# Kernel tuning notes

Hardware: AMD Instinct MI355X
Metric: run time of the kernel (lower is better)

Reference implementation:

```python
import jax, jax.numpy as jnp
import numpy as np

PI = float(np.pi)
K_NEIGH = 10  # self.k = k + 1 with k=9


def xyz2sphere(xyz):
    # cartesian2polar: [rho, theta/pi, phi/(2pi)+0.5] along last dim
    rho = jnp.sqrt(jnp.sum(xyz * xyz, axis=-1, keepdims=True))
    rho_s = jnp.maximum(rho, 1e-8)
    theta = jnp.arccos(jnp.clip(xyz[..., 2:3] / rho_s, -1.0, 1.0)) / PI
    phi = jnp.arctan2(xyz[..., 1:2], xyz[..., 0:1]) / (2.0 * PI) + 0.5
    return jnp.concatenate([rho, theta, phi], axis=-1)


def group_by_umbrella(xyz, k):
    # xyz: [B,3,N] -> [B,N,K,3,3] umbrella triangles (K = k-1 neighbors)
    pts = jnp.transpose(xyz, (0, 2, 1))                       # [B,N,3]
    sq = jnp.sum(pts * pts, axis=-1)                          # [B,N]
    d = sq[:, :, None] + sq[:, None, :] - 2.0 * jnp.einsum('bnc,bmc->bnm', pts, pts)
    idx = jax.lax.top_k(-d, k)[1]                             # [B,N,k] nearest incl. self
    group = jax.vmap(lambda p, i: p[i])(pts, idx)[:, :, 1:]   # drop self -> [B,N,K,3]
    gnorm = group - pts[:, :, None, :]                        # centered neighbors
    phi = xyz2sphere(gnorm)[..., 2]                           # [B,N,K]
    order = jnp.argsort(phi, axis=-1)
    srt = jnp.take_along_axis(gnorm, order[..., None], axis=2)[:, :, :, None, :]  # [B,N,K,1,3]
    rolled = jnp.roll(srt, -1, axis=2)
    return jnp.concatenate([jnp.zeros_like(srt), srt, rolled], axis=3)  # [B,N,K,3,3]


def cal_normal(g):
    # g: [B,N,K,3(points),3(coord)] -> unit normals [B,N,K,3]
    v1 = g[..., 1, :] - g[..., 0, :]
    v2 = g[..., 2, :] - g[..., 0, :]
    n = jnp.cross(v1, v2)
    nrm = jnp.sqrt(jnp.sum(n * n, axis=-1, keepdims=True))
    un = n / jnp.maximum(nrm, 1e-10)
    pos = jnp.where(un[..., 0:1, 0] > 0, 1.0, -1.0)[..., None]  # per-group sign fix
    return un * pos


def bn(x, g, b, m, v, eps=1e-5):
    # inference-mode BatchNorm2d over channel dim of [B,C,K,N]
    inv = g / jnp.sqrt(v + eps)
    return x * inv[:, None, None] + (b - m * inv)[:, None, None]


def conv1x1(x, w, b=None):
    y = jnp.einsum('oc,bckn->bokn', w, x)
    return y if b is None else y + b[:, None, None]


def setup_inputs() -> dict:
    key = jax.random.key(0)
    ks = jax.random.split(key, 16)
    C = 9
    return {
        'x': jax.random.normal(ks[0], (8, 3, 4096), dtype=jnp.float32),
        'conv1_w': jax.random.normal(ks[1], (C, C), dtype=jnp.float32) * 0.3,
        'bn1_g': jax.random.uniform(ks[2], (C,), dtype=jnp.float32) + 0.5,
        'bn1_b': jax.random.normal(ks[3], (C,), dtype=jnp.float32) * 0.1,
        'bn1_m': jax.random.normal(ks[4], (C,), dtype=jnp.float32) * 0.1,
        'bn1_v': jax.random.uniform(ks[5], (C,), dtype=jnp.float32) + 0.5,
        'conv2_w': jax.random.normal(ks[6], (C, C), dtype=jnp.float32) * 0.3,
        'conv2_b': jax.random.normal(ks[7], (C,), dtype=jnp.float32) * 0.1,
        'bn2_g': jax.random.uniform(ks[8], (C,), dtype=jnp.float32) + 0.5,
        'bn2_b': jax.random.normal(ks[9], (C,), dtype=jnp.float32) * 0.1,
        'bn2_m': jax.random.normal(ks[10], (C,), dtype=jnp.float32) * 0.1,
        'bn2_v': jax.random.uniform(ks[11], (C,), dtype=jnp.float32) + 0.5,
        'conv3_w': jax.random.normal(ks[12], (C, C), dtype=jnp.float32) * 0.3,
        'conv3_b': jax.random.normal(ks[13], (C,), dtype=jnp.float32) * 0.1,
    }


def reference(x, conv1_w, bn1_g, bn1_b, bn1_m, bn1_v, conv2_w, conv2_b,
              bn2_g, bn2_b, bn2_m, bn2_v, conv3_w, conv3_b):
    xyz = x[:, :3, :]
    gp = group_by_umbrella(xyz, K_NEIGH)                      # [B,N,K,3,3]
    normal = jnp.nan_to_num(cal_normal(gp))                   # [B,N,K,3]
    center = jnp.nan_to_num(jnp.mean(gp, axis=-2))            # [B,N,K,3]
    polar = xyz2sphere(center)                                # [B,N,K,3]
    feat = jnp.concatenate([center, polar, normal], axis=-1)  # [B,N,K,9]
    feat = jnp.transpose(feat, (0, 3, 2, 1))                  # [B,9,K,N]
    h = jax.nn.relu(bn(conv1x1(feat, conv1_w), bn1_g, bn1_b, bn1_m, bn1_v))
    h = jax.nn.relu(bn(conv1x1(h, conv2_w, conv2_b), bn2_g, bn2_b, bn2_m, bn2_v))
    h = conv1x1(h, conv3_w, conv3_b)
    return jnp.sum(h, axis=2)                                 # aggregation='sum' -> [B,9,N]
```

## Files before the change

kernel.cpp:

```cpp
#include <hip/hip_runtime.h>
#include <math.h>

#define NB 8
#define NP 4096
#define TOPK 10
#define KNB 9
#define QPB 16
#define SLC 8
#define NT 4
#define TPTS 1024
#define QPT (TPTS / SLC)
#define QW 132
#define CHW (SLC * QW)
#define MST (SLC * TOPK + 1)

#define FINF 3.0e38f
#define PI_F 3.14159274101257324f

__global__ __launch_bounds__(128, 4)
void repsurf_fused(const float* __restrict__ x,
                   const float* __restrict__ cw1,
                   const float* __restrict__ bg1, const float* __restrict__ bb1,
                   const float* __restrict__ bm1, const float* __restrict__ bv1,
                   const float* __restrict__ cw2, const float* __restrict__ cb2,
                   const float* __restrict__ bg2, const float* __restrict__ bb2,
                   const float* __restrict__ bm2, const float* __restrict__ bv2,
                   const float* __restrict__ cw3, const float* __restrict__ cb3,
                   float* __restrict__ out)
{
    __shared__ __align__(16) float uS[3 * CHW];
    float* md   = uS;
    int*   mi   = (int*)(uS + QPB * MST);
    float* tile = uS;

    __shared__ __align__(16) float sW1[9 * 12];
    __shared__ __align__(16) float sW2[9 * 12];
    __shared__ __align__(16) float sW3[9 * 12];
    __shared__ float sSh1[9], sSh2[9], sSh3[9];

    const int t  = threadIdx.x;
    const int b  = blockIdx.x >> 8;
    const int qc = blockIdx.x & 255;
    const float* xb = x + (size_t)b * 3 * NP;

    if (t < 108) {
        int o = t / 12, c = t % 12;
        float w1v = 0.f, w2v = 0.f, w3v = 0.f;
        if (c < 9) {
            float iv1 = bg1[o] * rsqrtf(bv1[o] + 1e-5f);
            float iv2 = bg2[o] * rsqrtf(bv2[o] + 1e-5f);
            w1v = cw1[o * 9 + c] * iv1;
            w2v = cw2[o * 9 + c] * iv2;
            w3v = cw3[o * 9 + c];
        }
        sW1[t] = w1v; sW2[t] = w2v; sW3[t] = w3v;
        if (t < 9) {
            float iv1 = bg1[t] * rsqrtf(bv1[t] + 1e-5f);
            float iv2 = bg2[t] * rsqrtf(bv2[t] + 1e-5f);
            sSh1[t] = bb1[t] - bm1[t] * iv1;
            sSh2[t] = cb2[t] * iv2 + bb2[t] - bm2[t] * iv2;
            sSh3[t] = cb3[t];
        }
    }

    const int q  = t & (QPB - 1);
    const int s  = t >> 4;
    const int qi = qc * QPB + q;
    const float qx = xb[qi], qy = xb[NP + qi], qz = xb[2 * NP + qi];

    float dk[TOPK];
    int   ik[TOPK];
#pragma unroll
    for (int j = 0; j < TOPK; ++j) { dk[j] = FINF; ik[j] = 0x7fffffff; }

    float db0 = 0.f, db1 = 0.f;
    int   ib0 = 0,   ib1 = 0,   cnt = 0;

#define INSERTE(DD, II) do { \
        float _d = (DD); int _i = (II); \
        if (_d < dk[TOPK - 1]) { \
            dk[TOPK - 1] = _d; ik[TOPK - 1] = _i; \
            _Pragma("unroll") \
            for (int jj = TOPK - 1; jj > 0; --jj) { \
                if (dk[jj] < dk[jj - 1]) { \
                    float td = dk[jj]; dk[jj] = dk[jj - 1]; dk[jj - 1] = td; \
                    int ti = ik[jj]; ik[jj] = ik[jj - 1]; ik[jj - 1] = ti; } \
            } \
        } } while (0)

#define DRAIN() do { \
        if (cnt >= 2) INSERTE(db1, ib1); \
        if (cnt >= 1) INSERTE(db0, ib0); \
        cnt = 0; } while (0)

#define DOCAND(PX, PY, PZ, MIDX) do { \
        float dx = (PX) - qx, dy = (PY) - qy, dz = (PZ) - qz; \
        float d = fmaf(dx, dx, fmaf(dy, dy, dz * dz)); \
        if (d < dk[TOPK - 1]) { db1 = db0; ib1 = ib0; db0 = d; ib0 = (MIDX); cnt++; } \
        if (__any(cnt >= 2)) DRAIN(); \
    } while (0)

    for (int tt = 0; tt < NT; ++tt) {
        const float* src0 = xb + tt * TPTS;
#pragma unroll
        for (int r = 0; r < 6; ++r) {
            int f = r * 128 + t;
            int c = f >> 8;
            int o = f & 255;
            float4 v = *(const float4*)(src0 + c * NP + o * 4);
            ((float4*)tile)[c * 264 + (o >> 5) * 33 + (o & 31)] = v;
        }
        __syncthreads();

        const float4* tx4 = (const float4*)tile + s * 33;
        const float4* ty4 = (const float4*)tile + 264 + s * 33;
        const float4* tz4 = (const float4*)tile + 528 + s * 33;
        const int base_idx = tt * TPTS + s * QPT;
        for (int mm = 0; mm < QPT / 4; ++mm) {
            float4 X = tx4[mm];
            float4 Y = ty4[mm];
            float4 Z = tz4[mm];
            const int m0 = base_idx + mm * 4;
            DOCAND(X.x, Y.x, Z.x, m0 + 0);
            DOCAND(X.y, Y.y, Z.y, m0 + 1);
            DOCAND(X.z, Y.z, Z.z, m0 + 2);
            DOCAND(X.w, Y.w, Z.w, m0 + 3);
        }
        __syncthreads();
    }
    DRAIN();

    const int qb = q * MST;
#pragma unroll
    for (int j = 0; j < TOPK; ++j) {
        md[qb + s * TOPK + j] = dk[j];
        mi[qb + s * TOPK + j] = ik[j];
    }
    __syncthreads();

    if (t < QPB) {
        int ni[KNB];
        int p0 = 0, p1 = 0, p2 = 0, p3 = 0, p4 = 0, p5 = 0, p6 = 0, p7 = 0;
#pragma unroll
        for (int j = 0; j < TOPK; ++j) {
#define GETH(K) float d##K; int i##K; \
            { int pk = p##K; \
              if (pk < TOPK) { d##K = md[qb + K * TOPK + pk]; i##K = mi[qb + K * TOPK + pk]; } \
              else { d##K = FINF; i##K = 0x7fffffff; } }
            GETH(0) GETH(1) GETH(2) GETH(3) GETH(4) GETH(5) GETH(6) GETH(7)
#undef GETH
#define WIN(DA, IA, SA, DB, IB, SB, DO_, IO_, SO_) \
            bool w_##SO_ = ((DA) < (DB)) || ((DA) == (DB) && (IA) < (IB)); \
            float DO_ = w_##SO_ ? (DA) : (DB); \
            int IO_ = w_##SO_ ? (IA) : (IB); \
            int SO_ = w_##SO_ ? (SA) : (SB);
            WIN(d0, i0, 0, d1, i1, 1, dA, iA, sA)
            WIN(d2, i2, 2, d3, i3, 3, dB, iB, sB)
            WIN(d4, i4, 4, d5, i5, 5, dC, iC, sC)
            WIN(d6, i6, 6, d7, i7, 7, dD, iD, sD)
            WIN(dA, iA, sA, dB, iB, sB, dE, iE, sE)
            WIN(dC, iC, sC, dD, iD, sD, dF, iF, sF)
            WIN(dE, iE, sE, dF, iF, sF, dG, iG, sw)
            (void)dG; (void)iG;
#undef WIN
            if (j > 0) ni[j - 1] = iG;
            p0 += (sw == 0); p1 += (sw == 1); p2 += (sw == 2); p3 += (sw == 3);
            p4 += (sw == 4); p5 += (sw == 5); p6 += (sw == 6); p7 += (sw == 7);
        }

        float gx[KNB], gy[KNB], gz[KNB], kk[KNB];
#pragma unroll
        for (int j = 0; j < KNB; ++j) {
            int id = ni[j];
            gx[j] = xb[id] - qx;
            gy[j] = xb[NP + id] - qy;
            gz[j] = xb[2 * NP + id] - qz;
            kk[j] = atan2f(gy[j], gx[j]);
        }
#pragma unroll
        for (int pass = 0; pass < KNB - 1; ++pass) {
#pragma unroll
            for (int j = 0; j < KNB - 1 - pass; ++j) {
                if (kk[j + 1] < kk[j]) {
                    float tv;
                    tv = kk[j]; kk[j] = kk[j + 1]; kk[j + 1] = tv;
                    tv = gx[j]; gx[j] = gx[j + 1]; gx[j + 1] = tv;
                    tv = gy[j]; gy[j] = gy[j + 1]; gy[j + 1] = tv;
                    tv = gz[j]; gz[j] = gz[j + 1]; gz[j + 1] = tv;
                }
            }
        }

        float ux[KNB], uy[KNB], uz[KNB];
#pragma unroll
        for (int j = 0; j < KNB; ++j) {
            int j2 = (j + 1 == KNB) ? 0 : j + 1;
            float nx_ = gy[j] * gz[j2] - gz[j] * gy[j2];
            float ny_ = gz[j] * gx[j2] - gx[j] * gz[j2];
            float nz_ = gx[j] * gy[j2] - gy[j] * gx[j2];
            float l = sqrtf(nx_ * nx_ + ny_ * ny_ + nz_ * nz_);
            float inv = 1.0f / fmaxf(l, 1e-10f);
            ux[j] = nx_ * inv; uy[j] = ny_ * inv; uz[j] = nz_ * inv;
        }
        float sgn = (ux[0] > 0.0f) ? 1.0f : -1.0f;

        const float4* W1v = (const float4*)sW1;
        const float4* W2v = (const float4*)sW2;
        const float4* W3v = (const float4*)sW3;

#define DOT9(WV, O, V) ( \
        (WV)[(O)*3+0].x * (V)[0] + (WV)[(O)*3+0].y * (V)[1] + \
        (WV)[(O)*3+0].z * (V)[2] + (WV)[(O)*3+0].w * (V)[3] + \
        (WV)[(O)*3+1].x * (V)[4] + (WV)[(O)*3+1].y * (V)[5] + \
        (WV)[(O)*3+1].z * (V)[6] + (WV)[(O)*3+1].w * (V)[7] + \
        (WV)[(O)*3+2].x * (V)[8] )

        float acc[9];
#pragma unroll
        for (int o = 0; o < 9; ++o) acc[o] = 0.0f;

#pragma unroll
        for (int j = 0; j < KNB; ++j) {
            int j2 = (j + 1 == KNB) ? 0 : j + 1;
            float cx = (gx[j] + gx[j2]) * (1.0f / 3.0f);
            float cy = (gy[j] + gy[j2]) * (1.0f / 3.0f);
            float cz = (gz[j] + gz[j2]) * (1.0f / 3.0f);
            float rho = sqrtf(cx * cx + cy * cy + cz * cz);
            float rs  = fmaxf(rho, 1e-8f);
            float ct  = fminf(fmaxf(cz / rs, -1.0f), 1.0f);
            float th  = acosf(ct) / PI_F;
            float ph  = atan2f(cy, cx) / (2.0f * PI_F) + 0.5f;
            float f[9]  = {cx, cy, cz, rho, th, ph, ux[j] * sgn, uy[j] * sgn, uz[j] * sgn};
            float t1[9], t2[9];
#pragma unroll
            for (int o = 0; o < 9; ++o)
                t1[o] = fmaxf(DOT9(W1v, o, f) + sSh1[o], 0.0f);
#pragma unroll
            for (int o = 0; o < 9; ++o)
                t2[o] = fmaxf(DOT9(W2v, o, t1) + sSh2[o], 0.0f);
#pragma unroll
            for (int o = 0; o < 9; ++o)
                acc[o] += DOT9(W3v, o, t2);
        }

        float* ob = out + (size_t)b * 9 * NP;
#pragma unroll
        for (int o = 0; o < 9; ++o)
            ob[o * NP + qi] = acc[o] + 9.0f * sSh3[o];
    }
}

extern "C" void kernel_launch(void* const* d_in, const int* in_sizes, int n_in,
                              void* d_out, int out_size, void* d_ws, size_t ws_size,
                              hipStream_t stream) {
    const float* x   = (const float*)d_in[0];
    const float* cw1 = (const float*)d_in[1];
    const float* bg1 = (const float*)d_in[2];
    const float* bb1 = (const float*)d_in[3];
    const float* bm1 = (const float*)d_in[4];
    const float* bv1 = (const float*)d_in[5];
    const float* cw2 = (const float*)d_in[6];
    const float* cb2 = (const float*)d_in[7];
    const float* bg2 = (const float*)d_in[8];
    const float* bb2 = (const float*)d_in[9];
    const float* bm2 = (const float*)d_in[10];
    const float* bv2 = (const float*)d_in[11];
    const float* cw3 = (const float*)d_in[12];
    const float* cb3 = (const float*)d_in[13];
    float* out = (float*)d_out;

    hipLaunchKernelGGL(repsurf_fused, dim3(NB * (NP / QPB)), dim3(128), 0, stream,
                       x, cw1, bg1, bb1, bm1, bv1, cw2, cb2, bg2, bb2, bm2, bv2,
                       cw3, cb3, out);
}
```

Measured before the change: 236.3 us.

## Replace branchy kNN insertion with two-pass branchless threshold then filtered insert

```diff
diff --git a/kernel.cpp b/kernel.cpp
--- a/kernel.cpp
+++ b/kernel.cpp
@@ -10,29 +10,25 @@
 #define NT 4
 #define TPTS 1024
 #define QPT (TPTS / SLC)
-#define QW 132
-#define CHW (SLC * QW)
+#define TSTR 129
 #define MST (SLC * TOPK + 1)
 
 #define FINF 3.0e38f
 #define PI_F 3.14159274101257324f
 
 __global__ __launch_bounds__(128, 4)
-void repsurf_fused(const float* __restrict__ x,
-                   const float* __restrict__ cw1,
-                   const float* __restrict__ bg1, const float* __restrict__ bb1,
-                   const float* __restrict__ bm1, const float* __restrict__ bv1,
-                   const float* __restrict__ cw2, const float* __restrict__ cb2,
-                   const float* __restrict__ bg2, const float* __restrict__ bb2,
-                   const float* __restrict__ bm2, const float* __restrict__ bv2,
-                   const float* __restrict__ cw3, const float* __restrict__ cb3,
-                   float* __restrict__ out)
+void repsurf_knn(const float* __restrict__ x,
+                 const float* __restrict__ cw1,
+                 const float* __restrict__ bg1, const float* __restrict__ bb1,
+                 const float* __restrict__ bm1, const float* __restrict__ bv1,
+                 const float* __restrict__ cw2, const float* __restrict__ cb2,
+                 const float* __restrict__ bg2, const float* __restrict__ bb2,
+                 const float* __restrict__ bm2, const float* __restrict__ bv2,
+                 const float* __restrict__ cw3, const float* __restrict__ cb3,
+                 float* __restrict__ out)
 {
-    __shared__ __align__(16) float uS[3 * CHW];
-    float* md   = uS;
-    int*   mi   = (int*)(uS + QPB * MST);
-    float* tile = uS;
-
+    __shared__ __align__(16) float4 tile[SLC * TSTR];
+    __shared__ float thrLds[128];
     __shared__ __align__(16) float sW1[9 * 12];
     __shared__ __align__(16) float sW2[9 * 12];
     __shared__ __align__(16) float sW3[9 * 12];
@@ -68,77 +64,99 @@
     const int qi = qc * QPB + q;
     const float qx = xb[qi], qy = xb[NP + qi], qz = xb[2 * NP + qi];
 
+#define DIST(P) fmaf((P).x - qx, (P).x - qx, fmaf((P).y - qy, (P).y - qy, ((P).z - qz) * ((P).z - qz)))
+
+#define CH1(P) do { \
+        float _d = DIST(P); \
+        _Pragma("unroll") \
+        for (int jj = TOPK - 1; jj > 0; --jj) \
+            dk[jj] = fminf(dk[jj], fmaxf(dk[jj - 1], _d)); \
+        dk[0] = fminf(dk[0], _d); } while (0)
+
     float dk[TOPK];
-    int   ik[TOPK];
-#pragma unroll
-    for (int j = 0; j < TOPK; ++j) { dk[j] = FINF; ik[j] = 0x7fffffff; }
-
-    float db0 = 0.f, db1 = 0.f;
-    int   ib0 = 0,   ib1 = 0,   cnt = 0;
-
-#define INSERTE(DD, II) do { \
+#pragma unroll
+    for (int j = 0; j < TOPK; ++j) dk[j] = FINF;
+
+    for (int tt = 0; tt < NT; ++tt) {
+        __syncthreads();
+        for (int i = t; i < TPTS; i += 128) {
+            int ss = i >> 7, m = i & 127;
+            int c = tt * TPTS + i;
+            tile[ss * TSTR + m] = make_float4(xb[c], xb[NP + c], xb[2 * NP + c], 0.f);
+        }
+        __syncthreads();
+        const float4* ts = tile + s * TSTR;
+        for (int g = 0; g < QPT / 4; ++g) {
+            float4 P0 = ts[g * 4 + 0];
+            float4 P1 = ts[g * 4 + 1];
+            float4 P2 = ts[g * 4 + 2];
+            float4 P3 = ts[g * 4 + 3];
+            CH1(P0); CH1(P1); CH1(P2); CH1(P3);
+        }
+    }
+
+    thrLds[t] = dk[TOPK - 1];
+    __syncthreads();
+    float T = thrLds[q];
+#pragma unroll
+    for (int ss = 1; ss < SLC; ++ss) T = fminf(T, thrLds[ss * QPB + q]);
+
+    float sk[TOPK];
+    int   si[TOPK];
+#pragma unroll
+    for (int j = 0; j < TOPK; ++j) { sk[j] = FINF; si[j] = 0x7fffffff; }
+
+#define INSERTP(DD, II) do { \
         float _d = (DD); int _i = (II); \
-        if (_d < dk[TOPK - 1]) { \
-            dk[TOPK - 1] = _d; ik[TOPK - 1] = _i; \
+        if (_d < sk[TOPK - 1]) { \
+            sk[TOPK - 1] = _d; si[TOPK - 1] = _i; \
             _Pragma("unroll") \
             for (int jj = TOPK - 1; jj > 0; --jj) { \
-                if (dk[jj] < dk[jj - 1]) { \
-                    float td = dk[jj]; dk[jj] = dk[jj - 1]; dk[jj - 1] = td; \
-                    int ti = ik[jj]; ik[jj] = ik[jj - 1]; ik[jj - 1] = ti; } \
+                if (sk[jj] < sk[jj - 1]) { \
+                    float td = sk[jj]; sk[jj] = sk[jj - 1]; sk[jj - 1] = td; \
+                    int ti = si[jj]; si[jj] = si[jj - 1]; si[jj - 1] = ti; } \
             } \
         } } while (0)
 
-#define DRAIN() do { \
-        if (cnt >= 2) INSERTE(db1, ib1); \
-        if (cnt >= 1) INSERTE(db0, ib0); \
-        cnt = 0; } while (0)
-
-#define DOCAND(PX, PY, PZ, MIDX) do { \
-        float dx = (PX) - qx, dy = (PY) - qy, dz = (PZ) - qz; \
-        float d = fmaf(dx, dx, fmaf(dy, dy, dz * dz)); \
-        if (d < dk[TOPK - 1]) { db1 = db0; ib1 = ib0; db0 = d; ib0 = (MIDX); cnt++; } \
-        if (__any(cnt >= 2)) DRAIN(); \
-    } while (0)
+#define CH2(P, IDX) do { \
+        float _dd = DIST(P); \
+        if (_dd <= T) INSERTP(_dd, (IDX)); } while (0)
 
     for (int tt = 0; tt < NT; ++tt) {
-        const float* src0 = xb + tt * TPTS;
-#pragma unroll
-        for (int r = 0; r < 6; ++r) {
-            int f = r * 128 + t;
-            int c = f >> 8;
-            int o = f & 255;
-            float4 v = *(const float4*)(src0 + c * NP + o * 4);
-            ((float4*)tile)[c * 264 + (o >> 5) * 33 + (o & 31)] = v;
-        }
-        __syncthreads();
-
-        const float4* tx4 = (const float4*)tile + s * 33;
-        const float4* ty4 = (const float4*)tile + 264 + s * 33;
-        const float4* tz4 = (const float4*)tile + 528 + s * 33;
-        const int base_idx = tt * TPTS + s * QPT;
-        for (int mm = 0; mm < QPT / 4; ++mm) {
-            float4 X = tx4[mm];
-            float4 Y = ty4[mm];
-            float4 Z = tz4[mm];
-            const int m0 = base_idx + mm * 4;
-            DOCAND(X.x, Y.x, Z.x, m0 + 0);
-            DOCAND(X.y, Y.y, Z.y, m0 + 1);
-            DOCAND(X.z, Y.z, Z.z, m0 + 2);
-            DOCAND(X.w, Y.w, Z.w, m0 + 3);
-        }
-        __syncthreads();
-    }
-    DRAIN();
-
-    const int qb = q * MST;
+        __syncthreads();
+        for (int i = t; i < TPTS; i += 128) {
+            int ss = i >> 7, m = i & 127;
+            int c = tt * TPTS + i;
+            tile[ss * TSTR + m] = make_float4(xb[c], xb[NP + c], xb[2 * NP + c], 0.f);
+        }
+        __syncthreads();
+        const float4* ts = tile + s * TSTR;
+        const int cb = tt * TPTS + s * QPT;
+        for (int g = 0; g < QPT / 4; ++g) {
+            float4 P0 = ts[g * 4 + 0];
+            float4 P1 = ts[g * 4 + 1];
+            float4 P2 = ts[g * 4 + 2];
+            float4 P3 = ts[g * 4 + 3];
+            CH2(P0, cb + g * 4 + 0);
+            CH2(P1, cb + g * 4 + 1);
+            CH2(P2, cb + g * 4 + 2);
+            CH2(P3, cb + g * 4 + 3);
+        }
+    }
+    __syncthreads();
+
+    float* md = (float*)tile;
+    int*   mi = (int*)((float*)tile + QPB * MST);
+    const int mb = q * MST + s * TOPK;
 #pragma unroll
     for (int j = 0; j < TOPK; ++j) {
-        md[qb + s * TOPK + j] = dk[j];
-        mi[qb + s * TOPK + j] = ik[j];
+        md[mb + j] = sk[j];
+        mi[mb + j] = si[j];
     }
     __syncthreads();
 
     if (t < QPB) {
+        const int qb = t * MST;
         int ni[KNB];
         int p0 = 0, p1 = 0, p2 = 0, p3 = 0, p4 = 0, p5 = 0, p6 = 0, p7 = 0;
 #pragma unroll
@@ -198,8 +216,8 @@
             float nx_ = gy[j] * gz[j2] - gz[j] * gy[j2];
             float ny_ = gz[j] * gx[j2] - gx[j] * gz[j2];
             float nz_ = gx[j] * gy[j2] - gy[j] * gx[j2];
-            float l = sqrtf(nx_ * nx_ + ny_ * ny_ + nz_ * nz_);
-            float inv = 1.0f / fmaxf(l, 1e-10f);
+            float ln = sqrtf(nx_ * nx_ + ny_ * ny_ + nz_ * nz_);
+            float inv = 1.0f / fmaxf(ln, 1e-10f);
             ux[j] = nx_ * inv; uy[j] = ny_ * inv; uz[j] = nz_ * inv;
         }
         float sgn = (ux[0] > 0.0f) ? 1.0f : -1.0f;
@@ -269,7 +287,7 @@
     const float* cb3 = (const float*)d_in[13];
     float* out = (float*)d_out;
 
-    hipLaunchKernelGGL(repsurf_fused, dim3(NB * (NP / QPB)), dim3(128), 0, stream,
+    hipLaunchKernelGGL(repsurf_knn, dim3(NB * (NP / QPB)), dim3(128), 0, stream,
                        x, cw1, bg1, bb1, bm1, bv1, cw2, cb2, bg2, bb2, bm2, bv2,
                        cw3, cb3, out);
 }
```

New measurement: 349.4 us. +47.9%, slower.
